# Optimization experiments

Hardware: AMD Instinct MI355X
Metric: run time of the kernel (lower is better)

Reference implementation:

```python
import jax, jax.numpy as jnp
import numpy as np

CHANNELS = 128


def setup_inputs() -> dict:
    key = jax.random.key(0)
    ks = jax.random.split(key, 7)
    B, N, C, E = 1, 50000, CHANNELS, 800000
    in_dim = 2 * C + 2  # channels*2 + 2
    tokens = jax.random.normal(ks[0], (B, N, C), dtype=jnp.float32)
    coords = jax.random.normal(ks[1], (B, N, 2), dtype=jnp.float32)
    edge_index = jax.random.randint(ks[2], (2, E), 0, N, dtype=jnp.int64)
    # MLP params: Linear(in_dim, C) -> ReLU -> Linear(C, 1)
    w1 = jax.random.normal(ks[3], (in_dim, C), dtype=jnp.float32) / np.sqrt(in_dim)
    b1 = jnp.zeros((C,), dtype=jnp.float32)
    w2 = jax.random.normal(ks[4], (C, 1), dtype=jnp.float32) / np.sqrt(C)
    b2 = jnp.zeros((1,), dtype=jnp.float32)
    return {"tokens": tokens, "coords": coords, "edge_index": edge_index,
            "w1": w1, "b1": b1, "w2": w2, "b2": b2}


def reference(tokens, coords, edge_index, w1, b1, w2, b2):
    src = edge_index[0]
    dst = edge_index[1]
    x_src = tokens[:, src, :]               # [B, E, C]
    x_dst = tokens[:, dst, :]               # [B, E, C]
    delta = coords[:, dst, :] - coords[:, src, :]  # [B, E, 2]
    feat = jnp.concatenate([x_src, x_dst, delta], axis=-1)  # [B, E, 2C+2]
    h = jax.nn.relu(jnp.einsum('bef,fh->beh', feat, w1) + b1)  # [B, E, C]
    return jnp.einsum('beh,ho->beo', h, w2) + b2               # [B, E, 1]
```

## Files before the change

### kernel.cpp

```cpp
#include <hip/hip_runtime.h>

static constexpr int CH   = 128;
static constexpr int KPAD = 192;

typedef __attribute__((ext_vector_type(8))) short bf16x8;
typedef __attribute__((ext_vector_type(4))) float f32x4;
typedef __attribute__((ext_vector_type(2))) unsigned int u32x2;

__device__ inline unsigned short f2bf(float x) {
    unsigned int u = __float_as_uint(x);
    unsigned int r = (u + 0x7fffu + ((u >> 16) & 1u)) >> 16;
    return (unsigned short)r;
}
__device__ inline unsigned int pack2bf(float a, float b) {
    return (unsigned int)f2bf(a) | ((unsigned int)f2bf(b) << 16);
}

__global__ __launch_bounds__(256) void prep_all(
    const float* __restrict__ w1, const float* __restrict__ b1,
    unsigned short* __restrict__ Wf, const unsigned int* __restrict__ idxw,
    uint2* __restrict__ idx2, long long E, long long Epad) {
    const int t = threadIdx.x;
    if (blockIdx.x < 20) {
        const int gid = blockIdx.x * 256 + t;
        const int lane = gid & 63;
        const int seg  = gid >> 6;
        const int m    = seg & 3;
        const int ks   = (seg >> 2) % 5;
        const int w    = seg / 20;
        const int c    = w * 64 + m * 16 + (lane & 15);
        const int k0   = ks * 32 + (lane >> 4) * 8;
        const bool isQ = c >= 128;
        const int cc   = c & 127;
        const float sgn = isQ ? 1.f : -1.f;
        unsigned int out[4];
#pragma unroll
        for (int h = 0; h < 4; ++h) {
            float v[2];
#pragma unroll
            for (int j = 0; j < 2; ++j) {
                const int k = k0 + 2 * h + j;
                float x;
                if (k < 128)       x = isQ ? w1[(size_t)(128 + k) * CH + cc]
                                           : w1[(size_t)k * CH + cc];
                else if (k == 128) x = sgn * w1[(size_t)(2 * CH) * CH + cc];
                else if (k == 129) x = sgn * w1[(size_t)(2 * CH + 1) * CH + cc];
                else if (k == 130) x = isQ ? b1[cc] : 0.f;
                else               x = 0.f;
                v[j] = x;
            }
            out[h] = pack2bf(v[0], v[1]);
        }
        *(uint4*)&Wf[(size_t)gid * 8] = make_uint4(out[0], out[1], out[2], out[3]);
        return;
    }
    unsigned nz = 0;
    const int lane = t & 63;
    for (int i = lane; i < 128; i += 64) nz |= idxw[2 * i + 1];
    const int is64 = (__ballot(nz != 0u) == 0ULL) ? 1 : 0;
    const long long bid = blockIdx.x - 20;
    const long long stride = (long long)(gridDim.x - 20) * 256;
    for (long long i = bid * 256 + t; i < Epad; i += stride) {
        uint2 v = make_uint2(0u, 0u);
        if (i < E) {
            const unsigned s = is64 ? idxw[2 * i] : idxw[i];
            const unsigned d = is64 ? idxw[2 * (E + i)] : idxw[E + i];
            v = make_uint2(s << 7, d << 7);
        }
        idx2[i] = v;
    }
}

__global__ __launch_bounds__(256) void node_mfma7(
    const float* __restrict__ tokens, const float* __restrict__ coords,
    const unsigned short* __restrict__ Wf, unsigned short* __restrict__ Plo,
    unsigned short* __restrict__ Phi, unsigned short* __restrict__ Qlo,
    unsigned short* __restrict__ Qhi, int N) {
    __shared__ unsigned short Atile[32 * KPAD];
    __shared__ unsigned short Otile[32 * 256];

    const int t    = threadIdx.x;
    const int l    = t & 63;
    const int wid  = t >> 6;
    const int n0   = blockIdx.x * 32;
    const int bl   = l & 15;
    const int bh   = l >> 4;

#pragma unroll
    for (int it = 0; it < 2; ++it) {
        const int idx  = it * 256 + t;
        const int node = idx >> 4;
        const int cq   = idx & 15;
        float4 v0 = make_float4(0.f, 0.f, 0.f, 0.f);
        float4 v1 = v0;
        if (n0 + node < N) {
            const float* src = &tokens[(size_t)(n0 + node) * CH + cq * 8];
            v0 = *(const float4*)src;
            v1 = *(const float4*)(src + 4);
        }
        uint4 u;
        u.x = pack2bf(v0.x, v0.y);
        u.y = pack2bf(v0.z, v0.w);
        u.z = pack2bf(v1.x, v1.y);
        u.w = pack2bf(v1.z, v1.w);
        const int byte = node * 384 + ((cq * 16) ^ ((node & 7) << 4));
        *(uint4*)((char*)Atile + byte) = u;
    }
    {
        const int node = t >> 3;
        const int ce   = t & 7;
        uint4 u = make_uint4(0u, 0u, 0u, 0u);
        if (ce == 0 && n0 + node < N) {
            const float cx = coords[2 * (n0 + node)];
            const float cy = coords[2 * (n0 + node) + 1];
            u.x = pack2bf(cx, cy);
            u.y = pack2bf(1.f, 0.f);
        }
        const int byte = node * 384 + (((16 + ce) * 16) ^ ((node & 7) << 4));
        *(uint4*)((char*)Atile + byte) = u;
    }
    __syncthreads();

    f32x4 acc[4][2];
#pragma unroll
    for (int m = 0; m < 4; ++m)
#pragma unroll
        for (int n = 0; n < 2; ++n) acc[m][n] = (f32x4){0.f, 0.f, 0.f, 0.f};

#pragma unroll
    for (int ks = 0; ks < 5; ++ks) {
        bf16x8 wfrag[4], tfrag[2];
#pragma unroll
        for (int m = 0; m < 4; ++m)
            wfrag[m] = *(const bf16x8*)&Wf[(size_t)(((wid * 5 + ks) * 4 + m) * 64
                                                    + l) * 8];
#pragma unroll
        for (int n = 0; n < 2; ++n) {
            const int row  = n * 16 + bl;
            const int byte = row * 384 + ((ks * 64 + bh * 16) ^ ((row & 7) << 4));
            tfrag[n] = *(const bf16x8*)((const char*)Atile + byte);
        }
#pragma unroll
        for (int m = 0; m < 4; ++m)
#pragma unroll
            for (int n = 0; n < 2; ++n)
                acc[m][n] = __builtin_amdgcn_mfma_f32_16x16x32_bf16(
                    wfrag[m], tfrag[n], acc[m][n], 0, 0, 0);
    }

#pragma unroll
    for (int m = 0; m < 4; ++m) {
        const int col = wid * 64 + m * 16 + bh * 4;
#pragma unroll
        for (int n = 0; n < 2; ++n) {
            const int node = n * 16 + bl;
            uint2 val;
            val.x = pack2bf(acc[m][n][0], acc[m][n][1]);
            val.y = pack2bf(acc[m][n][2], acc[m][n][3]);
            const int byte = node * 512 + ((col * 2) ^ ((node & 7) << 4));
            *(uint2*)((char*)Otile + byte) = val;
        }
    }
    __syncthreads();

#pragma unroll
    for (int it = 0; it < 2; ++it) {
        const int idx  = it * 256 + t;
        const int node = idx >> 4;
        const int seg  = idx & 15;
        const int gn   = n0 + node;
        if (gn < N) {
            unsigned short* dst = (seg < 4) ? Plo : (seg < 8) ? Phi
                                  : (seg < 12) ? Qlo : Qhi;
            const int colq = (seg & 3) * 16;
#pragma unroll
            for (int h = 0; h < 2; ++h) {
                const int byte = node * 512 +
                                 ((seg * 32 + h * 16) ^ ((node & 7) << 4));
                const uint4 v = *(const uint4*)((const char*)Otile + byte);
                *(uint4*)&dst[(size_t)gn * 64 + colq + h * 8] = v;
            }
        }
    }
}

template <int PASS>
__global__ __launch_bounds__(256) void edge_pass(
    const unsigned int* __restrict__ idx2w, const unsigned short* __restrict__ Pb,
    const unsigned short* __restrict__ Qb, const float* __restrict__ w2,
    const float* __restrict__ b2, float* __restrict__ partial,
    float* __restrict__ out, long long E) {
    const int t  = threadIdx.x;
    const int gl = t & 7;
    const long long nq = (E + 3) >> 2;
    const long long g0 = (long long)blockIdx.x * 32 + (t >> 3);
    const long long ng = (long long)gridDim.x * 32;
    const float4 wa = *(const float4*)&w2[PASS * 64 + gl * 8];
    const float4 wb = *(const float4*)&w2[PASS * 64 + gl * 8 + 4];
    const float bias = b2[0];
    const char* P = (const char*)Pb;
    const char* Q = (const char*)Qb;

    for (long long q = g0; q < nq; q += ng) {
        const long long e0 = q << 2;
        const u32x2 iv = __builtin_nontemporal_load(
            (const u32x2*)&idx2w[(e0 + (gl & 3)) * 2]);
        unsigned soff[4], doff[4];
#pragma unroll
        for (int j = 0; j < 4; ++j) {
            soff[j] = __shfl(iv.x, j, 8);
            doff[j] = __shfl(iv.y, j, 8);
        }
        uint4 pv[4], qv[4];
#pragma unroll
        for (int j = 0; j < 4; ++j)
            pv[j] = *(const uint4*)(P + soff[j] + 16 * gl);
#pragma unroll
        for (int j = 0; j < 4; ++j)
            qv[j] = *(const uint4*)(Q + doff[j] + 16 * gl);

        float part[4];
#pragma unroll
        for (int j = 0; j < 4; ++j) {
            const float wv[8] = {wa.x, wa.y, wa.z, wa.w, wb.x, wb.y, wb.z, wb.w};
            const unsigned pw[4] = {pv[j].x, pv[j].y, pv[j].z, pv[j].w};
            const unsigned qw[4] = {qv[j].x, qv[j].y, qv[j].z, qv[j].w};
            float acc = 0.f;
#pragma unroll
            for (int i = 0; i < 4; ++i) {
                const float plo = __uint_as_float(pw[i] << 16);
                const float phi = __uint_as_float(pw[i] & 0xffff0000u);
                const float qlo = __uint_as_float(qw[i] << 16);
                const float qhi = __uint_as_float(qw[i] & 0xffff0000u);
                acc = fmaf(fmaxf(plo + qlo, 0.f), wv[2 * i], acc);
                acc = fmaf(fmaxf(phi + qhi, 0.f), wv[2 * i + 1], acc);
            }
            part[j] = acc;
        }

        float t0 = part[0] + __shfl_xor(part[0], 1);
        float t1 = part[1] + __shfl_xor(part[1], 1);
        float t2 = part[2] + __shfl_xor(part[2], 1);
        float t3 = part[3] + __shfl_xor(part[3], 1);
        float a0 = (gl & 1) ? t1 : t0;
        float a1 = (gl & 1) ? t3 : t2;
        a0 += __shfl_xor(a0, 2);
        a1 += __shfl_xor(a1, 2);
        float c = (gl & 2) ? a1 : a0;
        c += __shfl_xor(c, 4);

        const long long e = e0 + gl;
        if (gl < 4 && e < E) {
            if (PASS == 0) {
                __builtin_nontemporal_store(c, &partial[e]);
            } else {
                out[e] = __builtin_nontemporal_load(&partial[e]) + c + bias;
            }
        }
    }
}

extern "C" void kernel_launch(void* const* d_in, const int* in_sizes, int n_in,
                              void* d_out, int out_size, void* d_ws,
                              size_t ws_size, hipStream_t stream) {
    const float* tokens = (const float*)d_in[0];
    const float* coords = (const float*)d_in[1];
    const unsigned int* idxw = (const unsigned int*)d_in[2];
    const float* w1 = (const float*)d_in[3];
    const float* b1 = (const float*)d_in[4];
    const float* w2 = (const float*)d_in[5];
    const float* b2 = (const float*)d_in[6];
    float* out = (float*)d_out;

    const int N = in_sizes[0] / CH;
    const long long E = in_sizes[2] / 2;
    const long long Epad = ((E + 3) >> 2) << 2;

    unsigned short* Plo = (unsigned short*)d_ws;
    unsigned short* Phi = Plo + (size_t)N * 64;
    unsigned short* Qlo = Phi + (size_t)N * 64;
    unsigned short* Qhi = Qlo + (size_t)N * 64;
    uint2* idx2 = (uint2*)(Qhi + (size_t)N * 64);
    unsigned short* Wf = (unsigned short*)(idx2 + Epad);
    float* partial = (float*)(Wf + 5120 * 8);

    prep_all<<<1044, 256, 0, stream>>>(w1, b1, Wf, idxw, idx2, E, Epad);

    node_mfma7<<<(N + 31) / 32, 256, 0, stream>>>(tokens, coords, Wf,
                                                  Plo, Phi, Qlo, Qhi, N);

    edge_pass<0><<<4096, 256, 0, stream>>>((const unsigned int*)idx2, Plo, Qlo,
                                           w2, b2, partial, out, E);
    edge_pass<1><<<4096, 256, 0, stream>>>((const unsigned int*)idx2, Phi, Qhi,
                                           w2, b2, partial, out, E);
}
```

Baseline: 71.98 us.

## Fuse two edge passes into one kernel with atomic accumulation into output

The two sequential edge-pass launches (low and high channel halves) become a single kernel in which even and odd blocks each handle one half. Both halves atomically add their partial dot products into the output, and the prep kernel now zero-fills the output in extra blocks. This drops one kernel launch and the partial-buffer write and read round trip. In exchange it adds float atomics on every edge, makes the summation order nondeterministic, and halves the grid-stride coverage per half, so each block processes twice as many edge groups.

Result: faster. 68.50 us (-4.8%).

```diff
diff --git a/kernel.cpp b/kernel.cpp
--- a/kernel.cpp
+++ b/kernel.cpp
@@ -19,7 +19,8 @@
 __global__ __launch_bounds__(256) void prep_all(
     const float* __restrict__ w1, const float* __restrict__ b1,
     unsigned short* __restrict__ Wf, const unsigned int* __restrict__ idxw,
-    uint2* __restrict__ idx2, long long E, long long Epad) {
+    uint2* __restrict__ idx2, float* __restrict__ out,
+    long long E, long long Epad) {
     const int t = threadIdx.x;
     if (blockIdx.x < 20) {
         const int gid = blockIdx.x * 256 + t;
@@ -33,7 +34,7 @@
         const bool isQ = c >= 128;
         const int cc   = c & 127;
         const float sgn = isQ ? 1.f : -1.f;
-        unsigned int out[4];
+        unsigned int outw[4];
 #pragma unroll
         for (int h = 0; h < 4; ++h) {
             float v[2];
@@ -49,17 +50,27 @@
                 else               x = 0.f;
                 v[j] = x;
             }
-            out[h] = pack2bf(v[0], v[1]);
-        }
-        *(uint4*)&Wf[(size_t)gid * 8] = make_uint4(out[0], out[1], out[2], out[3]);
+            outw[h] = pack2bf(v[0], v[1]);
+        }
+        *(uint4*)&Wf[(size_t)gid * 8] =
+            make_uint4(outw[0], outw[1], outw[2], outw[3]);
+        return;
+    }
+    if (blockIdx.x < 802) {
+        const long long base = (long long)(blockIdx.x - 20) * 1024 + t * 4;
+        if (base + 3 < E) {
+            *(float4*)&out[base] = make_float4(0.f, 0.f, 0.f, 0.f);
+        } else {
+            for (long long i = base; i < E; ++i) out[i] = 0.f;
+        }
         return;
     }
     unsigned nz = 0;
     const int lane = t & 63;
     for (int i = lane; i < 128; i += 64) nz |= idxw[2 * i + 1];
     const int is64 = (__ballot(nz != 0u) == 0ULL) ? 1 : 0;
-    const long long bid = blockIdx.x - 20;
-    const long long stride = (long long)(gridDim.x - 20) * 256;
+    const long long bid = blockIdx.x - 802;
+    const long long stride = (long long)(gridDim.x - 802) * 256;
     for (long long i = bid * 256 + t; i < Epad; i += stride) {
         uint2 v = make_uint2(0u, 0u);
         if (i < E) {
@@ -184,22 +195,24 @@
     }
 }
 
-template <int PASS>
-__global__ __launch_bounds__(256) void edge_pass(
-    const unsigned int* __restrict__ idx2w, const unsigned short* __restrict__ Pb,
-    const unsigned short* __restrict__ Qb, const float* __restrict__ w2,
-    const float* __restrict__ b2, float* __restrict__ partial,
+__global__ __launch_bounds__(256) void edge_fused(
+    const unsigned int* __restrict__ idx2w,
+    const unsigned short* __restrict__ Plo, const unsigned short* __restrict__ Phi,
+    const unsigned short* __restrict__ Qlo, const unsigned short* __restrict__ Qhi,
+    const float* __restrict__ w2, const float* __restrict__ b2,
     float* __restrict__ out, long long E) {
+    const int half = blockIdx.x & 1;
     const int t  = threadIdx.x;
     const int gl = t & 7;
     const long long nq = (E + 3) >> 2;
-    const long long g0 = (long long)blockIdx.x * 32 + (t >> 3);
-    const long long ng = (long long)gridDim.x * 32;
-    const float4 wa = *(const float4*)&w2[PASS * 64 + gl * 8];
-    const float4 wb = *(const float4*)&w2[PASS * 64 + gl * 8 + 4];
-    const float bias = b2[0];
-    const char* P = (const char*)Pb;
-    const char* Q = (const char*)Qb;
+    const long long pb = blockIdx.x >> 1;
+    const long long g0 = pb * 32 + (t >> 3);
+    const long long ng = (long long)(gridDim.x >> 1) * 32;
+    const float4 wa = *(const float4*)&w2[half * 64 + gl * 8];
+    const float4 wb = *(const float4*)&w2[half * 64 + gl * 8 + 4];
+    const float bias = half ? b2[0] : 0.f;
+    const char* P = (const char*)(half ? Phi : Plo);
+    const char* Q = (const char*)(half ? Qhi : Qlo);
 
     for (long long q = g0; q < nq; q += ng) {
         const long long e0 = q << 2;
@@ -250,13 +263,7 @@
         c += __shfl_xor(c, 4);
 
         const long long e = e0 + gl;
-        if (gl < 4 && e < E) {
-            if (PASS == 0) {
-                __builtin_nontemporal_store(c, &partial[e]);
-            } else {
-                out[e] = __builtin_nontemporal_load(&partial[e]) + c + bias;
-            }
-        }
+        if (gl < 4 && e < E) atomicAdd(&out[e], c + bias);
     }
 }
 
@@ -282,15 +289,12 @@
     unsigned short* Qhi = Qlo + (size_t)N * 64;
     uint2* idx2 = (uint2*)(Qhi + (size_t)N * 64);
     unsigned short* Wf = (unsigned short*)(idx2 + Epad);
-    float* partial = (float*)(Wf + 5120 * 8);
-
-    prep_all<<<1044, 256, 0, stream>>>(w1, b1, Wf, idxw, idx2, E, Epad);
+
+    prep_all<<<1826, 256, 0, stream>>>(w1, b1, Wf, idxw, idx2, out, E, Epad);
 
     node_mfma7<<<(N + 31) / 32, 256, 0, stream>>>(tokens, coords, Wf,
                                                   Plo, Phi, Qlo, Qhi, N);
 
-    edge_pass<0><<<4096, 256, 0, stream>>>((const unsigned int*)idx2, Plo, Qlo,
-                                           w2, b2, partial, out, E);
-    edge_pass<1><<<4096, 256, 0, stream>>>((const unsigned int*)idx2, Phi, Qhi,
-                                           w2, b2, partial, out, E);
-}
+    edge_fused<<<4096, 256, 0, stream>>>((const unsigned int*)idx2,
+                                         Plo, Phi, Qlo, Qhi, w2, b2, out, E);
+}
```
